# Kernel tuning notes

Hardware: AMD Instinct MI355X
Metric: run time of the kernel (lower is better)

## Reference

```python
import jax, jax.numpy as jnp
import numpy as np
from jax import lax

N = 8192

def _conv(x, w, b):
    # x: NCHW, w: OIHW, valid conv stride 1
    y = lax.conv_general_dilated(x, w, (1, 1), 'VALID',
                                 dimension_numbers=('NCHW', 'OIHW', 'NCHW'))
    return y + b[None, :, None, None]

def _maxpool2(x):
    return lax.reduce_window(x, -jnp.inf, lax.max, (1, 1, 2, 2), (1, 1, 2, 2), 'VALID')

def setup_inputs() -> dict:
    key = jax.random.key(0)
    ks = jax.random.split(key, 13)
    def rn(k, shape, scale):
        return jax.random.normal(k, shape, dtype=jnp.float32) * scale
    inp = {}
    inp['x'] = jax.random.normal(ks[0], (N, 3, 32, 32), dtype=jnp.float32)
    inp['W1'] = rn(ks[1], (6, 3, 5, 5), 0.1)
    inp['b1'] = rn(ks[2], (6,), 0.1)
    inp['W2'] = rn(ks[3], (16, 6, 5, 5), 0.08)
    inp['b2'] = rn(ks[4], (16,), 0.1)
    inp['Wf1'] = rn(ks[5], (120, 400), 0.05)
    inp['bf1'] = rn(ks[6], (120,), 0.05)
    inp['Wf2'] = rn(ks[7], (84, 120), 0.09)
    inp['bf2'] = rn(ks[8], (84,), 0.09)
    inp['Wg'] = rn(ks[9], (10, 84), 0.1)    # GATConv fc weight (no bias)
    inp['attn_l'] = rn(ks[10], (10,), 0.3)  # a_l (src)
    inp['attn_r'] = rn(ks[11], (10,), 0.3)  # a_r (dst)
    inp['bg'] = rn(ks[12], (10,), 0.1)      # GATConv output bias
    return inp

def reference(x, W1, b1, W2, b2, Wf1, bf1, Wf2, bf2, Wg, attn_l, attn_r, bg):
    # CNN feature extractor (LeNet style)
    h = _maxpool2(jax.nn.relu(_conv(x, W1, b1)))   # [N,6,14,14]
    h = _maxpool2(jax.nn.relu(_conv(h, W2, b2)))   # [N,16,5,5]
    h = h.reshape(-1, 16 * 5 * 5)                  # [N,400]
    h = jax.nn.relu(h @ Wf1.T + bf1)               # [N,120]
    h = jax.nn.relu(h @ Wf2.T + bf2)               # [N,84]
    # Single-head GAT over fully-connected graph (incl. self-loops):
    # equivalent dense formulation of DGL GATConv(84,10,1)
    z = h @ Wg.T                                    # [N,10]
    el = z @ attn_l                                 # src scores [N]
    er = z @ attn_r                                 # dst scores [N]
    # e[i,j]: edge src=j -> dst=i
    e = jax.nn.leaky_relu(er[:, None] + el[None, :], negative_slope=0.2)  # [N,N]
    alpha = jax.nn.softmax(e, axis=1)               # softmax over incoming edges
    out = alpha @ z + bg                            # [N,10]
    return out
```

## Files before the change

kernel.cpp:

```cpp
#include <hip/hip_runtime.h>
#include <hip/hip_bf16.h>

typedef _Float16 half8 __attribute__((ext_vector_type(8)));
typedef __attribute__((aligned(8))) half8 half8_a8;
typedef float floatx4 __attribute__((ext_vector_type(4)));

#define LOG2E 1.44269504088896340736f

__device__ __forceinline__ float pool4_dpp(float v) {
  int s1 = __builtin_amdgcn_update_dpp(0, __float_as_int(v), 0xB1, 0xF, 0xF, true);
  float v1 = fmaxf(v, __int_as_float(s1));
  int s2 = __builtin_amdgcn_update_dpp(0, __float_as_int(v1), 0x4E, 0xF, 0xF, true);
  return fmaxf(v1, __int_as_float(s2));
}

__device__ __forceinline__ unsigned f2mono(float f) {
  unsigned u = __float_as_uint(f);
  return (u & 0x80000000u) ? ~u : (u | 0x80000000u);
}
__device__ __forceinline__ float mono2f(unsigned u) {
  return (u & 0x80000000u) ? __uint_as_float(u & 0x7fffffffu)
                           : __uint_as_float(~u);
}

__global__ __launch_bounds__(256) void k_prep(const float* __restrict__ Wf1,
    const float* __restrict__ Wf2, const float* __restrict__ Wg,
    const float* __restrict__ W1, const float* __restrict__ W2,
    _Float16* __restrict__ w1f, _Float16* __restrict__ w2f,
    _Float16* __restrict__ wgf, _Float16* __restrict__ B1,
    _Float16* __restrict__ B2M, unsigned* __restrict__ emx) {
  const int i = blockIdx.x * 256 + threadIdx.x;
  if (i == 0) emx[0] = 0u;
  if (i < 53248) {
    const int n = i / 416, k = i - n * 416;
    w1f[i] = (_Float16)((n < 120 && k < 400) ? Wf1[n * 400 + k] : 0.f);
  } else if (i < 65536) {
    const int j = i - 53248;
    const int n = j >> 7, k = j & 127;
    w2f[j] = (_Float16)((n < 84 && k < 120) ? Wf2[n * 120 + k] : 0.f);
  } else if (i < 67072) {
    const int g = i - 65536;
    const int n = g / 96, k = g - n * 96;
    wgf[g] = (_Float16)((n < 10 && k < 84) ? Wg[n * 84 + k] : 0.f);
  } else if (i < 73216) {
    const int g = i - 67072;
    const int n = g / 192, k = g - n * 192;
    const int co = n >> 2, cy = (n >> 1) & 1, cx = n & 1;
    const int pidx = k >> 3, j = k & 7;
    const int r = pidx >> 2, ci = pidx & 3;
    float v = 0.f;
    if (co < 6 && ci < 3) {
      const int ky = r - cy, kx = j - cx;
      if (ky >= 0 && ky < 5 && kx >= 0 && kx < 5)
        v = W1[((co * 3 + ci) * 5 + ky) * 5 + kx];
    }
    B1[g] = (_Float16)v;
  } else if (i < 77312) {
    const int g = i - 73216;
    const int n = g >> 8, k = g & 255;
    float v = 0.f;
    if (k < 240) {
      const int ci = k / 40, rem = k - ci * 40, r = rem >> 3, j = rem & 7;
      if (j < 5) v = W2[((n * 6 + ci) * 5 + r) * 5 + j];
    }
    B2M[g] = (_Float16)v;
  }
}

__global__ __launch_bounds__(256, 3) void k_convs(const float* __restrict__ x,
    const _Float16* __restrict__ B1, const float* __restrict__ b1,
    const _Float16* __restrict__ B2M, const float* __restrict__ b2,
    _Float16* __restrict__ h2) {
  __shared__ __align__(16) char sm[53712];
  _Float16* h1L = (_Float16*)(sm + 46656);
  const int t = threadIdx.x;
  const int n0 = blockIdx.x * 3;
  const int w4 = t >> 6, lane = t & 63;
  const int l16 = lane & 15, q = lane >> 4;

  half8 bfr1[2][6];
#pragma unroll
  for (int nt = 0; nt < 2; nt++)
#pragma unroll
    for (int kc = 0; kc < 6; kc++)
      bfr1[nt][kc] =
          *(const half8*)(B1 + (size_t)(nt * 16 + l16) * 192 + kc * 32 + q * 8);
  half8 bfr2[8];
#pragma unroll
  for (int kc = 0; kc < 8; kc++)
    bfr2[kc] = *(const half8*)(B2M + (size_t)l16 * 256 + kc * 32 + q * 8);
  const int co_n = l16 >> 2;
  const int co1 = 4 + co_n;
  const float bias1_0 = b1[co_n];
  const float bias1_1 = (co1 < 6) ? b1[co1] : 0.f;
  const float bias2 = b2[l16];

  const float4* x4 = (const float4*)(x + (size_t)n0 * 3072);
  for (int i = t; i < 2304; i += 256) {
    const int img = i / 768;
    float4 v = make_float4(0.f, 0.f, 0.f, 0.f);
    if (n0 + img < 8192) v = x4[i];
    const int ii = i - img * 768;
    const int ci = ii >> 8, rem2 = ii & 255;
    const int y = rem2 >> 3, c = rem2 & 7;
    union { _Float16 h[2]; unsigned u; } p01, p23;
    p01.h[0] = (_Float16)v.x; p01.h[1] = (_Float16)v.y;
    p23.h[0] = (_Float16)v.z; p23.h[1] = (_Float16)v.w;
    char* row = sm + img * 15552 + ci * 5184 + y * 80;
    *(uint2*)(row + 8 * c) = make_uint2(p01.u, p23.u);
    *(unsigned*)(row + 2596 + 8 * c) = p01.u;
    *(unsigned*)(row + 2600 + 8 * c) = p23.u;
  }
  if (t < 192) {
    const int img = t / 96, tt = t - img * 96;
    const int ci = tt >> 5, y = tt & 31;
    *(unsigned*)(sm + img * 15552 + ci * 5184 + 2596 + y * 80 + 64) = 0u;
    if (t < 96) {
      const int ci2 = t >> 5, y2 = t & 31;
      *(unsigned*)(sm + 2 * 15552 + ci2 * 5184 + 2596 + y2 * 80 + 64) = 0u;
    }
  }
  if (t < 48) {
    const int im = t >> 4;
    if (n0 + im < 8192)
      h2[(size_t)(n0 + im) * 416 + 400 + (t & 15)] = (_Float16)0.f;
  }
  __syncthreads();

  {
    const int px = l16;
    const int colOff = (px & 1) ? (2596 + 4 * px) : (4 * px);
    const char* cbase = sm + ((q == 3) ? 0 : q * 5184) + colOff;
    const bool store_lane = (l16 & 3) == 0;
    for (int u = w4; u < 42; u += 4) {
      const int img = u / 14, py = u - img * 14;
      const char* base = cbase + img * 15552;
      half8 a[6];
#pragma unroll
      for (int r = 0; r < 6; r++)
        a[r] = *(const half8_a8*)(base + (2 * py + r) * 80);
      floatx4 acc0, acc1;
#pragma unroll
      for (int r = 0; r < 4; r++) { acc0[r] = 0.f; acc1[r] = 0.f; }
#pragma unroll
      for (int kc = 0; kc < 6; kc++) {
        acc0 = __builtin_amdgcn_mfma_f32_16x16x32_f16(a[kc], bfr1[0][kc], acc0, 0, 0, 0);
        acc1 = __builtin_amdgcn_mfma_f32_16x16x32_f16(a[kc], bfr1[1][kc], acc1, 0, 0, 0);
      }
      float p0[4], p1[4];
#pragma unroll
      for (int r = 0; r < 4; r++) {
        p0[r] = fmaxf(pool4_dpp(acc0[r]) + bias1_0, 0.f);
        p1[r] = fmaxf(pool4_dpp(acc1[r]) + bias1_1, 0.f);
      }
      if (store_lane) {
        union { _Float16 h[2]; unsigned u; } s01, s23;
        s01.h[0] = (_Float16)p0[0]; s01.h[1] = (_Float16)p0[1];
        s23.h[0] = (_Float16)p0[2]; s23.h[1] = (_Float16)p0[3];
        _Float16* dst = h1L + img * 1176 + co_n * 196 + py * 14 + q * 4;
        *(unsigned*)dst = s01.u;
        if (q < 3) *(unsigned*)(dst + 2) = s23.u;
        if (co1 < 6) {
          union { _Float16 h[2]; unsigned u; } t01, t23;
          t01.h[0] = (_Float16)p1[0]; t01.h[1] = (_Float16)p1[1];
          t23.h[0] = (_Float16)p1[2]; t23.h[1] = (_Float16)p1[3];
          _Float16* dst1 = h1L + img * 1176 + co1 * 196 + py * 14 + q * 4;
          *(unsigned*)dst1 = t01.u;
          if (q < 3) *(unsigned*)(dst1 + 2) = t23.u;
        }
      }
    }
  }
  __syncthreads();

  for (int uu = t; uu < 504; uu += 256) {
    const int img = uu / 168, rem = uu - img * 168;
    const int ci = rem / 28, r2 = rem - ci * 28;
    const int y = r2 >> 1, g = r2 & 1;
    const unsigned* src = (const unsigned*)(h1L + img * 1176 + ci * 196 + y * 14);
    unsigned u6[6];
#pragma unroll
    for (int k = 0; k < 6; k++) {
      const int idx = 4 * g + k;
      u6[k] = (idx < 7) ? src[idx] : 0u;
    }
    char* base = sm + img * 11136 + ci * 1856 + y * 32 + 16 * g;
#pragma unroll
    for (int ww = 0; ww < 4; ww++) {
      *(unsigned*)(base + 4 * ww) = u6[ww];
      *(unsigned*)(base + 464 + 4 * ww) = (u6[ww] >> 16) | (u6[ww + 1] << 16);
      *(unsigned*)(base + 928 + 4 * ww) = u6[ww + 1];
      *(unsigned*)(base + 1392 + 4 * ww) = (u6[ww + 1] >> 16) | (u6[ww + 2] << 16);
    }
  }
  __syncthreads();

  {
    int C2[8];
#pragma unroll
    for (int kc = 0; kc < 8; kc++) {
      const int pidx = kc * 4 + q;
      C2[kc] = (pidx < 30) ? (pidx / 5) * 1856 + (pidx % 5) * 32 : 0;
    }
    for (int mt = w4; mt < 19; mt += 4) {
      const int m = min(mt * 16 + l16, 299);
      const int pos = m >> 2, cy = (m >> 1) & 1, cx = m & 1;
      const int img = pos / 25, p = pos - img * 25;
      const int py = p / 5, px = p - py * 5;
      const int h = 2 * px + cx, s = h & 3;
      const char* base =
          sm + img * 11136 + s * 464 + (2 * py + cy) * 32 + (h - s) * 2;
      half8 a[8];
#pragma unroll
      for (int kc = 0; kc < 8; kc++) a[kc] = *(const half8_a8*)(base + C2[kc]);
      floatx4 acc;
#pragma unroll
      for (int r = 0; r < 4; r++) acc[r] = 0.f;
#pragma unroll
      for (int kc = 0; kc < 8; kc++)
        acc = __builtin_amdgcn_mfma_f32_16x16x32_f16(a[kc], bfr2[kc], acc, 0, 0, 0);
      const float v = fmaxf(fmaxf(acc[0], acc[1]), fmaxf(acc[2], acc[3]));
      const int posL = mt * 4 + q;
      if (posL < 75) {
        const int im = posL / 25, pp = posL - im * 25;
        if (n0 + im < 8192)
          h2[(size_t)(n0 + im) * 416 + l16 * 25 + pp] =
              (_Float16)fmaxf(v + bias2, 0.f);
      }
    }
  }
}

__global__ __launch_bounds__(256) void k_mlp(
    const _Float16* __restrict__ h2, const _Float16* __restrict__ w1,
    const float* __restrict__ bf1, const _Float16* __restrict__ w2,
    const float* __restrict__ bf2, const _Float16* __restrict__ wg,
    const float* __restrict__ al, const float* __restrict__ ar,
    _Float16* __restrict__ zT, float* __restrict__ el, float* __restrict__ er,
    unsigned* __restrict__ emx) {
  __shared__ __align__(16) _Float16 h3s[32 * 136];
  __shared__ __align__(16) _Float16 h4s[32 * 104];
  __shared__ float zs[32 * 17];
  const int t = threadIdx.x;
  const int w = t >> 6, lane = t & 63;
  const int l16 = lane & 15, q = lane >> 4;
  const int row0 = blockIdx.x * 32;
  for (int i = t; i < 2176; i += 256) ((float*)h3s)[i] = 0.f;
  for (int i = t; i < 1664; i += 256) ((float*)h4s)[i] = 0.f;
  const int rt = w & 1, cg = w >> 1;
  const int am = row0 + rt * 16 + l16;
  floatx4 acc[4];
#pragma unroll
  for (int ct = 0; ct < 4; ct++)
#pragma unroll
    for (int r = 0; r < 4; r++) acc[ct][r] = 0.f;
  const half8* Ag = (const half8*)(h2 + (size_t)am * 416 + q * 8);
  for (int kc = 0; kc < 13; kc++) {
    half8 a = Ag[kc * 4];
#pragma unroll
    for (int ct = 0; ct < 4; ct++) {
      const int n = cg * 64 + ct * 16 + l16;
      half8 b = *(const half8*)(w1 + (size_t)n * 416 + kc * 32 + q * 8);
      acc[ct] = __builtin_amdgcn_mfma_f32_16x16x32_f16(a, b, acc[ct], 0, 0, 0);
    }
  }
  __syncthreads();
#pragma unroll
  for (int ct = 0; ct < 4; ct++) {
    const int n = cg * 64 + ct * 16 + l16;
    if (n < 120) {
      const float bias = bf1[n];
#pragma unroll
      for (int r = 0; r < 4; r++) {
        const int rr = rt * 16 + q * 4 + r;
        h3s[rr * 136 + n] = (_Float16)fmaxf(acc[ct][r] + bias, 0.f);
      }
    }
  }
  __syncthreads();
  const int cbase2 = (w >> 1) * 3;
  floatx4 acc2[3];
#pragma unroll
  for (int ct = 0; ct < 3; ct++)
#pragma unroll
    for (int r = 0; r < 4; r++) acc2[ct][r] = 0.f;
  const _Float16* A2 = h3s + (rt * 16 + l16) * 136 + q * 8;
  for (int kc = 0; kc < 4; kc++) {
    half8 a = *(const half8*)(A2 + kc * 32);
#pragma unroll
    for (int ct = 0; ct < 3; ct++) {
      const int n = (cbase2 + ct) * 16 + l16;
      half8 b = *(const half8*)(w2 + (size_t)n * 128 + kc * 32 + q * 8);
      acc2[ct] = __builtin_amdgcn_mfma_f32_16x16x32_f16(a, b, acc2[ct], 0, 0, 0);
    }
  }
  __syncthreads();
#pragma unroll
  for (int ct = 0; ct < 3; ct++) {
    const int n = (cbase2 + ct) * 16 + l16;
    if (n < 84) {
      const float bias = bf2[n];
#pragma unroll
      for (int r = 0; r < 4; r++) {
        const int rr = rt * 16 + q * 4 + r;
        h4s[rr * 104 + n] = (_Float16)fmaxf(acc2[ct][r] + bias, 0.f);
      }
    }
  }
  __syncthreads();
  if (w < 2) {
    floatx4 acc3;
#pragma unroll
    for (int r = 0; r < 4; r++) acc3[r] = 0.f;
    const _Float16* A3 = h4s + (w * 16 + l16) * 104 + q * 8;
    for (int kc = 0; kc < 3; kc++) {
      half8 a = *(const half8*)(A3 + kc * 32);
      half8 b = *(const half8*)(wg + (size_t)l16 * 96 + kc * 32 + q * 8);
      acc3 = __builtin_amdgcn_mfma_f32_16x16x32_f16(a, b, acc3, 0, 0, 0);
    }
#pragma unroll
    for (int r = 0; r < 4; r++) {
      const int rr = w * 16 + q * 4 + r;
      zs[rr * 17 + l16] = acc3[r];
    }
  }
  __syncthreads();
  if (t < 32) {
    float e1 = 0.f, e2 = 0.f;
#pragma unroll
    for (int d = 0; d < 10; d++) {
      const float zv = zs[t * 17 + d];
      e1 += zv * al[d];
      e2 += zv * ar[d];
    }
    const float elv = e1 * LOG2E;
    el[row0 + t] = elv;
    er[row0 + t] = e2 * LOG2E;
    float m = elv;
#pragma unroll
    for (int off = 16; off > 0; off >>= 1)
      m = fmaxf(m, __shfl_down(m, off, 32));
    if (t == 0) atomicMax(emx, f2mono(m));
  }
  for (int idx = t; idx < 352; idx += 256) {
    const int d = idx >> 5, c = idx & 31;
    zT[(size_t)d * 8192 + row0 + c] =
        (d < 10) ? (_Float16)zs[c * 17 + d] : (_Float16)1.0f;
  }
}

__global__ __launch_bounds__(1024) void k_attn(const _Float16* __restrict__ zT,
    const float* __restrict__ el, const float* __restrict__ er,
    const unsigned* __restrict__ emx, const float* __restrict__ bg,
    float* __restrict__ out) {
  __shared__ float red[8][2][16][12];
  const int t = threadIdx.x;
  const int w = t >> 6, lane = t & 63;
  const int l16 = lane & 15, q = lane >> 4;
  const int isub = w & 1, js = w >> 1;
  const int row0 = blockIdx.x * 32;
  const int itile = row0 + isub * 16;
  const int jb = js * 1024;
  const float mx = mono2f(emx[0]);
  const float eri = er[itile + l16];
  const float s0 = eri + mx;
  const float mi = fmaxf(s0, 0.2f * s0);
  floatx4 acc;
#pragma unroll
  for (int r = 0; r < 4; r++) acc[r] = 0.f;
  const float* elp = el + jb + q * 8;
  const _Float16* ztp = zT + (size_t)l16 * 8192 + jb + q * 8;
  for (int jc = 0; jc < 32; jc++) {
    const float4 e0 = *(const float4*)(elp + jc * 32);
    const float4 e1 = *(const float4*)(elp + jc * 32 + 4);
    float wf[8];
    const float ej[8] = {e0.x, e0.y, e0.z, e0.w, e1.x, e1.y, e1.z, e1.w};
#pragma unroll
    for (int u = 0; u < 8; u++) {
      const float s = eri + ej[u];
      const float lr = fmaxf(s, 0.2f * s);
      wf[u] = exp2f(lr - mi);
    }
    half8 a;
#pragma unroll
    for (int u = 0; u < 8; u++) a[u] = (_Float16)wf[u];
    const half8 b = *(const half8*)(ztp + jc * 32);
    acc = __builtin_amdgcn_mfma_f32_16x16x32_f16(a, b, acc, 0, 0, 0);
  }
  if (l16 < 11) {
#pragma unroll
    for (int r = 0; r < 4; r++) red[js][isub][q * 4 + r][l16] = acc[r];
  }
  __syncthreads();
  if (t < 320) {
    const int ii = t / 10, d = t - (t / 10) * 10;
    const int i1 = ii >> 4, i2 = ii & 15;
    float num = 0.f, den = 0.f;
#pragma unroll
    for (int s = 0; s < 8; s++) {
      num += red[s][i1][i2][d];
      den += red[s][i1][i2][10];
    }
    out[(size_t)(row0 + ii) * 10 + d] = num / den + bg[d];
  }
}

extern "C" void kernel_launch(void* const* d_in, const int* in_sizes, int n_in,
                              void* d_out, int out_size, void* d_ws, size_t ws_size,
                              hipStream_t stream) {
  const float* x   = (const float*)d_in[0];
  const float* W1  = (const float*)d_in[1];
  const float* b1  = (const float*)d_in[2];
  const float* W2  = (const float*)d_in[3];
  const float* b2  = (const float*)d_in[4];
  const float* Wf1 = (const float*)d_in[5];
  const float* bf1 = (const float*)d_in[6];
  const float* Wf2 = (const float*)d_in[7];
  const float* bf2 = (const float*)d_in[8];
  const float* Wg  = (const float*)d_in[9];
  const float* al  = (const float*)d_in[10];
  const float* ar  = (const float*)d_in[11];
  const float* bg  = (const float*)d_in[12];
  float* out = (float*)d_out;

  float* ws = (float*)d_ws;
  float* p = ws + (size_t)8192 * 588;
  _Float16* h2f = (_Float16*)p;
  p += (size_t)8192 * 208;
  _Float16* zTf = (_Float16*)p; p += 65536;
  float* el  = p; p += 8192;
  float* er  = p; p += 8192;
  unsigned* emx = (unsigned*)p; p += 16;
  _Float16* w1f = (_Float16*)p; p += 26624;
  _Float16* w2f = (_Float16*)p; p += 6144;
  _Float16* wgf = (_Float16*)p; p += 768;
  _Float16* B1g = (_Float16*)p; p += 3072;
  _Float16* B2g = (_Float16*)p; p += 2048;

  k_prep<<<302, 256, 0, stream>>>(Wf1, Wf2, Wg, W1, W2, w1f, w2f, wgf, B1g, B2g, emx);
  k_convs<<<2731, 256, 0, stream>>>(x, B1g, b1, B2g, b2, h2f);
  k_mlp<<<256, 256, 0, stream>>>(h2f, w1f, bf1, w2f, bf2, wgf, al, ar, zTf, el, er, emx);
  k_attn<<<256, 1024, 0, stream>>>(zTf, el, er, emx, bg, out);
}
```

Before: 261.7 us.

## Shrink conv LDS footprint and registers to raise occupancy, two images per block

The fused conv kernel now handles 2 images per block instead of 3 and drops the duplicated odd-column and four-way shifted LDS copies in favour of padded rows (68/36-byte strides) read with 4-byte loads. LDS falls from about 53.7KB to 17.8KB, and the launch bound rises from 3 to 8 blocks per CU. Conv1 now gives each wave one image half and slides a 6-row register window, reusing 4 of 6 rows per pooled output row. Conv2 reloads its B fragments from global memory inside the loop rather than keeping them in registers. The costs are more, narrower LDS reads, extra global and L2 traffic for the weights, and more blocks to schedule.

```diff
diff --git a/kernel.cpp b/kernel.cpp
--- a/kernel.cpp
+++ b/kernel.cpp
@@ -2,7 +2,6 @@
 #include <hip/hip_bf16.h>
 
 typedef _Float16 half8 __attribute__((ext_vector_type(8)));
-typedef __attribute__((aligned(8))) half8 half8_a8;
 typedef float floatx4 __attribute__((ext_vector_type(4)));
 
 #define LOG2E 1.44269504088896340736f
@@ -67,130 +66,116 @@
   }
 }
 
-__global__ __launch_bounds__(256, 3) void k_convs(const float* __restrict__ x,
+__global__ __launch_bounds__(256, 8) void k_convs(const float* __restrict__ x,
     const _Float16* __restrict__ B1, const float* __restrict__ b1,
     const _Float16* __restrict__ B2M, const float* __restrict__ b2,
     _Float16* __restrict__ h2) {
-  __shared__ __align__(16) char sm[53712];
-  _Float16* h1L = (_Float16*)(sm + 46656);
+  __shared__ __align__(16) char sm[17792];
+  _Float16* h1L = (_Float16*)(sm + 13088);
   const int t = threadIdx.x;
-  const int n0 = blockIdx.x * 3;
+  const int n0 = blockIdx.x * 2;
   const int w4 = t >> 6, lane = t & 63;
   const int l16 = lane & 15, q = lane >> 4;
 
-  half8 bfr1[2][6];
-#pragma unroll
-  for (int nt = 0; nt < 2; nt++)
-#pragma unroll
-    for (int kc = 0; kc < 6; kc++)
-      bfr1[nt][kc] =
-          *(const half8*)(B1 + (size_t)(nt * 16 + l16) * 192 + kc * 32 + q * 8);
-  half8 bfr2[8];
-#pragma unroll
-  for (int kc = 0; kc < 8; kc++)
-    bfr2[kc] = *(const half8*)(B2M + (size_t)l16 * 256 + kc * 32 + q * 8);
-  const int co_n = l16 >> 2;
-  const int co1 = 4 + co_n;
-  const float bias1_0 = b1[co_n];
-  const float bias1_1 = (co1 < 6) ? b1[co1] : 0.f;
-  const float bias2 = b2[l16];
-
   const float4* x4 = (const float4*)(x + (size_t)n0 * 3072);
-  for (int i = t; i < 2304; i += 256) {
-    const int img = i / 768;
-    float4 v = make_float4(0.f, 0.f, 0.f, 0.f);
-    if (n0 + img < 8192) v = x4[i];
+  for (int i = t; i < 1536; i += 256) {
+    const float4 v = x4[i];
+    const int img = (i >= 768);
     const int ii = i - img * 768;
     const int ci = ii >> 8, rem2 = ii & 255;
     const int y = rem2 >> 3, c = rem2 & 7;
     union { _Float16 h[2]; unsigned u; } p01, p23;
     p01.h[0] = (_Float16)v.x; p01.h[1] = (_Float16)v.y;
     p23.h[0] = (_Float16)v.z; p23.h[1] = (_Float16)v.w;
-    char* row = sm + img * 15552 + ci * 5184 + y * 80;
-    *(uint2*)(row + 8 * c) = make_uint2(p01.u, p23.u);
-    *(unsigned*)(row + 2596 + 8 * c) = p01.u;
-    *(unsigned*)(row + 2600 + 8 * c) = p23.u;
+    char* row = sm + img * 6544 + ci * 2180 + y * 68;
+    *(unsigned*)(row + 8 * c) = p01.u;
+    *(unsigned*)(row + 8 * c + 4) = p23.u;
   }
   if (t < 192) {
     const int img = t / 96, tt = t - img * 96;
     const int ci = tt >> 5, y = tt & 31;
-    *(unsigned*)(sm + img * 15552 + ci * 5184 + 2596 + y * 80 + 64) = 0u;
-    if (t < 96) {
-      const int ci2 = t >> 5, y2 = t & 31;
-      *(unsigned*)(sm + 2 * 15552 + ci2 * 5184 + 2596 + y2 * 80 + 64) = 0u;
-    }
-  }
-  if (t < 48) {
+    *(unsigned*)(sm + img * 6544 + ci * 2180 + y * 68 + 64) = 0u;
+  }
+  if (t < 32) {
     const int im = t >> 4;
-    if (n0 + im < 8192)
-      h2[(size_t)(n0 + im) * 416 + 400 + (t & 15)] = (_Float16)0.f;
+    h2[(size_t)(n0 + im) * 416 + 400 + (t & 15)] = (_Float16)0.f;
   }
   __syncthreads();
 
   {
-    const int px = l16;
-    const int colOff = (px & 1) ? (2596 + 4 * px) : (4 * px);
-    const char* cbase = sm + ((q == 3) ? 0 : q * 5184) + colOff;
+    const int img = w4 >> 1, wl = w4 & 1;
+    const char* base = sm + img * 6544 + ((q == 3) ? 0 : q * 2180) + 4 * l16;
+    const int py0 = wl * 7;
     const bool store_lane = (l16 & 3) == 0;
-    for (int u = w4; u < 42; u += 4) {
-      const int img = u / 14, py = u - img * 14;
-      const char* base = cbase + img * 15552;
-      half8 a[6];
-#pragma unroll
-      for (int r = 0; r < 6; r++)
-        a[r] = *(const half8_a8*)(base + (2 * py + r) * 80);
-      floatx4 acc0, acc1;
-#pragma unroll
-      for (int r = 0; r < 4; r++) { acc0[r] = 0.f; acc1[r] = 0.f; }
-#pragma unroll
-      for (int kc = 0; kc < 6; kc++) {
-        acc0 = __builtin_amdgcn_mfma_f32_16x16x32_f16(a[kc], bfr1[0][kc], acc0, 0, 0, 0);
-        acc1 = __builtin_amdgcn_mfma_f32_16x16x32_f16(a[kc], bfr1[1][kc], acc1, 0, 0, 0);
-      }
-      float p0[4], p1[4];
-#pragma unroll
-      for (int r = 0; r < 4; r++) {
-        p0[r] = fmaxf(pool4_dpp(acc0[r]) + bias1_0, 0.f);
-        p1[r] = fmaxf(pool4_dpp(acc1[r]) + bias1_1, 0.f);
-      }
-      if (store_lane) {
-        union { _Float16 h[2]; unsigned u; } s01, s23;
-        s01.h[0] = (_Float16)p0[0]; s01.h[1] = (_Float16)p0[1];
-        s23.h[0] = (_Float16)p0[2]; s23.h[1] = (_Float16)p0[3];
-        _Float16* dst = h1L + img * 1176 + co_n * 196 + py * 14 + q * 4;
-        *(unsigned*)dst = s01.u;
-        if (q < 3) *(unsigned*)(dst + 2) = s23.u;
-        if (co1 < 6) {
-          union { _Float16 h[2]; unsigned u; } t01, t23;
-          t01.h[0] = (_Float16)p1[0]; t01.h[1] = (_Float16)p1[1];
-          t23.h[0] = (_Float16)p1[2]; t23.h[1] = (_Float16)p1[3];
-          _Float16* dst1 = h1L + img * 1176 + co1 * 196 + py * 14 + q * 4;
-          *(unsigned*)dst1 = t01.u;
-          if (q < 3) *(unsigned*)(dst1 + 2) = t23.u;
+    for (int nt = 0; nt < 2; nt++) {
+      const int co = nt * 4 + (l16 >> 2);
+      half8 bfr[6];
+#pragma unroll
+      for (int kc = 0; kc < 6; kc++)
+        bfr[kc] = *(const half8*)(B1 + (size_t)(nt * 16 + l16) * 192 + kc * 32 + q * 8);
+      const float bias = (co < 6) ? b1[co] : 0.f;
+      union AU { unsigned u[4]; half8 h; } a[6];
+#pragma unroll
+      for (int r = 0; r < 6; r++) {
+        const char* rp = base + (2 * py0 + r) * 68;
+        a[r].u[0] = *(const unsigned*)(rp);
+        a[r].u[1] = *(const unsigned*)(rp + 4);
+        a[r].u[2] = *(const unsigned*)(rp + 8);
+        a[r].u[3] = *(const unsigned*)(rp + 12);
+      }
+      for (int py = py0; py < py0 + 7; ++py) {
+        floatx4 acc;
+#pragma unroll
+        for (int r = 0; r < 4; r++) acc[r] = 0.f;
+#pragma unroll
+        for (int kc = 0; kc < 6; kc++)
+          acc = __builtin_amdgcn_mfma_f32_16x16x32_f16(a[kc].h, bfr[kc], acc, 0, 0, 0);
+        if (py < py0 + 6) {
+          a[0] = a[2]; a[1] = a[3]; a[2] = a[4]; a[3] = a[5];
+          const char* rp4 = base + (2 * py + 6) * 68;
+          a[4].u[0] = *(const unsigned*)(rp4);
+          a[4].u[1] = *(const unsigned*)(rp4 + 4);
+          a[4].u[2] = *(const unsigned*)(rp4 + 8);
+          a[4].u[3] = *(const unsigned*)(rp4 + 12);
+          const char* rp5 = rp4 + 68;
+          a[5].u[0] = *(const unsigned*)(rp5);
+          a[5].u[1] = *(const unsigned*)(rp5 + 4);
+          a[5].u[2] = *(const unsigned*)(rp5 + 8);
+          a[5].u[3] = *(const unsigned*)(rp5 + 12);
         }
-      }
-    }
-  }
-  __syncthreads();
-
-  for (int uu = t; uu < 504; uu += 256) {
+        float p0[4];
+#pragma unroll
+        for (int r = 0; r < 4; r++)
+          p0[r] = fmaxf(pool4_dpp(acc[r]) + bias, 0.f);
+        if (store_lane && co < 6) {
+          union { _Float16 h[2]; unsigned u; } s01, s23;
+          s01.h[0] = (_Float16)p0[0]; s01.h[1] = (_Float16)p0[1];
+          s23.h[0] = (_Float16)p0[2]; s23.h[1] = (_Float16)p0[3];
+          _Float16* dst = h1L + img * 1176 + co * 196 + py * 14 + q * 4;
+          *(unsigned*)dst = s01.u;
+          if (q < 3) *(unsigned*)(dst + 2) = s23.u;
+        }
+      }
+    }
+  }
+  __syncthreads();
+
+  for (int uu = t; uu < 336; uu += 256) {
     const int img = uu / 168, rem = uu - img * 168;
     const int ci = rem / 28, r2 = rem - ci * 28;
     const int y = r2 >> 1, g = r2 & 1;
     const unsigned* src = (const unsigned*)(h1L + img * 1176 + ci * 196 + y * 14);
-    unsigned u6[6];
-#pragma unroll
-    for (int k = 0; k < 6; k++) {
+    unsigned u5[5];
+#pragma unroll
+    for (int k = 0; k < 5; k++) {
       const int idx = 4 * g + k;
-      u6[k] = (idx < 7) ? src[idx] : 0u;
-    }
-    char* base = sm + img * 11136 + ci * 1856 + y * 32 + 16 * g;
-#pragma unroll
-    for (int ww = 0; ww < 4; ww++) {
-      *(unsigned*)(base + 4 * ww) = u6[ww];
-      *(unsigned*)(base + 464 + 4 * ww) = (u6[ww] >> 16) | (u6[ww + 1] << 16);
-      *(unsigned*)(base + 928 + 4 * ww) = u6[ww + 1];
-      *(unsigned*)(base + 1392 + 4 * ww) = (u6[ww + 1] >> 16) | (u6[ww + 2] << 16);
+      u5[k] = (idx < 7) ? src[idx] : 0u;
+    }
+    char* b0 = sm + img * 6544 + ci * 1016 + y * 36 + 16 * g;
+#pragma unroll
+    for (int w = 0; w < 4; w++) {
+      *(unsigned*)(b0 + 4 * w) = u5[w];
+      *(unsigned*)(b0 + 508 + 4 * w) = (u5[w] >> 16) | (u5[w + 1] << 16);
     }
   }
   __syncthreads();
@@ -200,32 +185,36 @@
 #pragma unroll
     for (int kc = 0; kc < 8; kc++) {
       const int pidx = kc * 4 + q;
-      C2[kc] = (pidx < 30) ? (pidx / 5) * 1856 + (pidx % 5) * 32 : 0;
-    }
-    for (int mt = w4; mt < 19; mt += 4) {
-      const int m = min(mt * 16 + l16, 299);
+      C2[kc] = (pidx < 30) ? (pidx / 5) * 1016 + (pidx % 5) * 36 : 0;
+    }
+    const float bias2 = b2[l16];
+    for (int mt = w4; mt < 13; mt += 4) {
+      const int m = min(mt * 16 + l16, 199);
       const int pos = m >> 2, cy = (m >> 1) & 1, cx = m & 1;
       const int img = pos / 25, p = pos - img * 25;
       const int py = p / 5, px = p - py * 5;
-      const int h = 2 * px + cx, s = h & 3;
       const char* base =
-          sm + img * 11136 + s * 464 + (2 * py + cy) * 32 + (h - s) * 2;
-      half8 a[8];
-#pragma unroll
-      for (int kc = 0; kc < 8; kc++) a[kc] = *(const half8_a8*)(base + C2[kc]);
+          sm + img * 6544 + cx * 508 + (2 * py + cy) * 36 + 4 * px;
       floatx4 acc;
 #pragma unroll
       for (int r = 0; r < 4; r++) acc[r] = 0.f;
 #pragma unroll
-      for (int kc = 0; kc < 8; kc++)
-        acc = __builtin_amdgcn_mfma_f32_16x16x32_f16(a[kc], bfr2[kc], acc, 0, 0, 0);
+      for (int kc = 0; kc < 8; kc++) {
+        union { unsigned u[4]; half8 h; } av;
+        const char* ap = base + C2[kc];
+        av.u[0] = *(const unsigned*)(ap);
+        av.u[1] = *(const unsigned*)(ap + 4);
+        av.u[2] = *(const unsigned*)(ap + 8);
+        av.u[3] = *(const unsigned*)(ap + 12);
+        const half8 bv = *(const half8*)(B2M + (size_t)l16 * 256 + kc * 32 + q * 8);
+        acc = __builtin_amdgcn_mfma_f32_16x16x32_f16(av.h, bv, acc, 0, 0, 0);
+      }
       const float v = fmaxf(fmaxf(acc[0], acc[1]), fmaxf(acc[2], acc[3]));
       const int posL = mt * 4 + q;
-      if (posL < 75) {
+      if (posL < 50) {
         const int im = posL / 25, pp = posL - im * 25;
-        if (n0 + im < 8192)
-          h2[(size_t)(n0 + im) * 416 + l16 * 25 + pp] =
-              (_Float16)fmaxf(v + bias2, 0.f);
+        h2[(size_t)(n0 + im) * 416 + l16 * 25 + pp] =
+            (_Float16)fmaxf(v + bias2, 0.f);
       }
     }
   }
@@ -438,7 +427,7 @@
   _Float16* B2g = (_Float16*)p; p += 2048;
 
   k_prep<<<302, 256, 0, stream>>>(Wf1, Wf2, Wg, W1, W2, w1f, w2f, wgf, B1g, B2g, emx);
-  k_convs<<<2731, 256, 0, stream>>>(x, B1g, b1, B2g, b2, h2f);
+  k_convs<<<4096, 256, 0, stream>>>(x, B1g, b1, B2g, b2, h2f);
   k_mlp<<<256, 256, 0, stream>>>(h2f, w1f, bf1, w2f, bf2, wgf, al, ar, zTf, el, er, emx);
   k_attn<<<256, 1024, 0, stream>>>(zTf, el, er, emx, bg, out);
 }
```

After: 279.5 us. 1.07x slower.
